# Optimization experiments

Measured on AMD Instinct MI355X. Metric: run time of the kernel, lower is better.

## Reference

```python
import jax, jax.numpy as jnp
import numpy as np

B, C, D, H, W = 4, 128, 16, 16, 16
INNER = 64  # channels // reduction


def setup_inputs() -> dict:
    key = jax.random.key(0)
    ks = jax.random.split(key, 4)
    s = 0.02
    return {
        "x": jax.random.normal(ks[0], (B, C, D, H, W), dtype=jnp.float32),
        "Wq": jax.random.normal(ks[1], (INNER, C), dtype=jnp.float32) * s,
        "bq": jnp.zeros((INNER,), dtype=jnp.float32),
        "Wk": jax.random.normal(ks[2], (INNER, C), dtype=jnp.float32) * s,
        "bk": jnp.zeros((INNER,), dtype=jnp.float32),
        "Wv": jax.random.normal(ks[3], (C, C), dtype=jnp.float32) * s,
        "bv": jnp.zeros((C,), dtype=jnp.float32),
        "gamma": jnp.zeros((1,), dtype=jnp.float32),
    }


def reference(x, Wq, bq, Wk, bk, Wv, bv, gamma):
    b, c, d, h, w = x.shape
    n = d * h * w
    inner = Wq.shape[0]
    scale = inner ** (-0.5)
    xf = x.reshape(b, c, n)  # flatten spatial dims
    # 1x1 Conv3d == per-position channel matmul
    q = jnp.einsum('oc,bcn->bon', Wq, xf) + bq[None, :, None]  # [B, inner, N]
    k = jnp.einsum('oc,bcn->bon', Wk, xf) + bk[None, :, None]  # [B, inner, N]
    v = jnp.einsum('oc,bcn->bon', Wv, xf) + bv[None, :, None]  # [B, C, N]
    # attn[b, n, m] = softmax_m(q[:, :, n] . k[:, :, m] * scale)
    attn = jax.nn.softmax(jnp.einsum('bon,bom->bnm', q, k) * scale, axis=-1)
    # out = v @ attn^T  -> out[b, c, n] = sum_m v[b, c, m] * attn[b, n, m]
    out = jnp.einsum('bcm,bnm->bcn', v, attn).reshape(b, c, d, h, w)
    return x + gamma[0] * out
```

## Files before the change

kernel.cpp:

```cpp
#include <hip/hip_runtime.h>
#include <cstdint>

#define B_ 4
#define C_ 128
#define INNER_ 64
#define N_ 4096
#define SPLITS 12
#define KT 32
#define TT 128

typedef __attribute__((ext_vector_type(8))) short short8;
typedef __attribute__((ext_vector_type(4))) short bf16x4;
typedef __attribute__((ext_vector_type(4))) float f32x4;
typedef __attribute__((ext_vector_type(2))) unsigned u32x2;

typedef const __attribute__((address_space(1))) void* gp_t;
typedef __attribute__((address_space(3))) void* lp_t;

__device__ __forceinline__ short f2bf(float f) {
  unsigned u = __builtin_bit_cast(unsigned, f);
  unsigned r = (u + 0x7FFFu + ((u >> 16) & 1u)) >> 16;
  return (short)r;
}
__device__ __forceinline__ float bf2f(short s) {
  return __builtin_bit_cast(float, ((unsigned)(unsigned short)s) << 16);
}
__device__ __forceinline__ float fexp2(float x) {
#if __has_builtin(__builtin_amdgcn_exp2f)
  return __builtin_amdgcn_exp2f(x);
#else
  return exp2f(x);
#endif
}
__device__ __forceinline__ unsigned pk2(float lo, float hi) {
#if __has_builtin(__builtin_amdgcn_cvt_pk_bf16_f32)
  typedef __attribute__((ext_vector_type(2))) __bf16 bfp;
  bfp v = __builtin_amdgcn_cvt_pk_bf16_f32(lo, hi);
  return __builtin_bit_cast(unsigned, v);
#else
  return (unsigned)(unsigned short)f2bf(lo) | ((unsigned)(unsigned short)f2bf(hi) << 16);
#endif
}

__device__ __forceinline__ f32x4 mfma16(bf16x4 a, bf16x4 b, f32x4 c) {
#if __has_builtin(__builtin_amdgcn_mfma_f32_16x16x16bf16_1k)
  return __builtin_amdgcn_mfma_f32_16x16x16bf16_1k(a, b, c, 0, 0, 0);
#elif __has_builtin(__builtin_amdgcn_mfma_f32_16x16x16_bf16)
  return __builtin_amdgcn_mfma_f32_16x16x16_bf16(a, b, c, 0, 0, 0);
#else
  f32x4 d;
  asm volatile("v_mfma_f32_16x16x16_bf16 %0, %1, %2, %3"
               : "=v"(d) : "v"(a), "v"(b), "v"(c));
  return d;
#endif
}

__global__ __launch_bounds__(256) void pack_kernel(
    const float* __restrict__ Wq, const float* __restrict__ bq,
    const float* __restrict__ Wk, const float* __restrict__ bk,
    const float* __restrict__ Wv, const float* __restrict__ bv,
    short* __restrict__ wp, float* __restrict__ bp)
{
  const int idx = blockIdx.x * 256 + threadIdx.x;
  const int o = idx >> 7, c = idx & 127;
  float v;
  if (o < 64)       v = Wq[o * C_ + c];
  else if (o < 128) v = Wk[(o - 64) * C_ + c];
  else              v = Wv[(o - 128) * C_ + c];
  wp[idx] = f2bf(v);
  if (c == 0)
    bp[o] = (o < 64) ? bq[o] : (o < 128) ? bk[o - 64] : bv[o - 128];
}

__global__ __launch_bounds__(256) void qkv_kernel(
    const float* __restrict__ x, const short* __restrict__ wp,
    const float* __restrict__ bp,
    short* __restrict__ qg, short* __restrict__ kg, short* __restrict__ vg)
{
  __shared__ short xT[32 * 136];
  __shared__ short outb[256 * 40];
  __shared__ float biasL[256];

  const int tid = threadIdx.x;
  const int b   = blockIdx.x >> 7;
  const int n0  = (blockIdx.x & 127) << 5;
  const float QSC = 0.125f * 1.44269504088896340736f;

  biasL[tid] = bp[tid];
  const float* xb = x + (size_t)b * C_ * N_ + n0;
  for (int i = tid; i < 1024; i += 256) {
    const int c = i >> 3, seg = i & 7;
    const float4 v = *(const float4*)&xb[(size_t)c * N_ + seg * 4];
    xT[(seg * 4 + 0) * 136 + c] = f2bf(v.x);
    xT[(seg * 4 + 1) * 136 + c] = f2bf(v.y);
    xT[(seg * 4 + 2) * 136 + c] = f2bf(v.z);
    xT[(seg * 4 + 3) * 136 + c] = f2bf(v.w);
  }
  __syncthreads();

  const int w = tid >> 6, lane = tid & 63, quad = lane >> 4, l16 = lane & 15;

  short8 xf[2][4];
#pragma unroll
  for (int nt = 0; nt < 2; ++nt)
#pragma unroll
    for (int kk = 0; kk < 4; ++kk)
      xf[nt][kk] = *(const short8*)&xT[(nt * 16 + l16) * 136 + kk * 32 + quad * 8];

  if (w < 2) {
    const int obase = w * 64;
    const float osc = (w == 0) ? QSC : 1.0f;
#pragma unroll
    for (int ot = 0; ot < 4; ++ot) {
      const int o = obase + ot * 16 + l16;
      short8 wf[4];
#pragma unroll
      for (int kk = 0; kk < 4; ++kk)
        wf[kk] = *(const short8*)&wp[(size_t)o * 128 + kk * 32 + quad * 8];
      const float bias = biasL[o];
#pragma unroll
      for (int nt = 0; nt < 2; ++nt) {
        f32x4 acc = (f32x4){0.f, 0.f, 0.f, 0.f};
#pragma unroll
        for (int kk = 0; kk < 4; ++kk)
          acc = __builtin_amdgcn_mfma_f32_16x16x32_bf16(xf[nt][kk], wf[kk], acc, 0, 0, 0);
#pragma unroll
        for (int r = 0; r < 4; ++r)
          outb[o * 40 + nt * 16 + quad * 4 + r] = f2bf((acc[r] + bias) * osc);
      }
    }
  } else {
    const int ob2 = (w - 2) * 64;
#pragma unroll
    for (int ot = 0; ot < 4; ++ot) {
      const int orow = 128 + ob2 + ot * 16 + l16;
      short8 wf[4];
#pragma unroll
      for (int kk = 0; kk < 4; ++kk)
        wf[kk] = *(const short8*)&wp[(size_t)orow * 128 + kk * 32 + quad * 8];
#pragma unroll
      for (int nt = 0; nt < 2; ++nt) {
        f32x4 acc = (f32x4){0.f, 0.f, 0.f, 0.f};
#pragma unroll
        for (int kk = 0; kk < 4; ++kk)
          acc = __builtin_amdgcn_mfma_f32_16x16x32_bf16(wf[kk], xf[nt][kk], acc, 0, 0, 0);
#pragma unroll
        for (int r = 0; r < 4; ++r) {
          const int o_r = 128 + ob2 + ot * 16 + quad * 4 + r;
          outb[o_r * 40 + nt * 16 + l16] = f2bf(acc[r] + biasL[o_r]);
        }
      }
    }
  }
  __syncthreads();

  {
    const int n = tid >> 3, oc = tid & 7;
    short8 qv, kv;
#pragma unroll
    for (int j = 0; j < 8; ++j) {
      qv[j] = outb[(oc * 8 + j) * 40 + n];
      kv[j] = outb[(64 + oc * 8 + j) * 40 + n];
    }
    *(short8*)&qg[(((size_t)b * N_ + n0 + n) << 6) + oc * 8] = qv;
    *(short8*)&kg[(((size_t)b * N_ + n0 + n) << 6) + oc * 8] = kv;
  }
  {
    const int T = n0 >> 5;
#pragma unroll
    for (int rep = 0; rep < 2; ++rep) {
      const int idx2 = rep * 256 + tid;
      const int c0  = idx2 & 63;
      const int k4l = idx2 >> 6;
      const bf16x4 lo = *(const bf16x4*)&outb[(128 + 2 * c0) * 40 + k4l * 4];
      const bf16x4 hi = *(const bf16x4*)&outb[(128 + 2 * c0 + 1) * 40 + k4l * 4];
      short8 vv;
#pragma unroll
      for (int j = 0; j < 4; ++j) { vv[j] = lo[j]; vv[4 + j] = hi[j]; }
      const size_t tb = (((size_t)b * 128 + T) * 8 + k4l) * 512 + c0 * 8;
      *(short8*)&vg[tb] = vv;
    }
  }
}

__global__ __launch_bounds__(256, 4) void attn_kernel(
    const short* __restrict__ qb, const short* __restrict__ kb,
    const short* __restrict__ vb,
    short* __restrict__ Opart, float* __restrict__ lbuf)
{
  __shared__ short kbuf[2][2048];
  __shared__ short vbuf[2][4096];

  const int tid = threadIdx.x;
  const int bid = blockIdx.x;
  const int s   = bid % SPLITS;
  const int qt  = (bid / SPLITS) & 31;
  const int b   = bid / (SPLITS * 32);
  const int m0  = qt << 7;
  const int w   = tid >> 6, lane = tid & 63, quad = lane >> 4, l16 = lane & 15;
  const int rbase = m0 + w * 32;

  const int t0  = (s * TT) / SPLITS;
  const int NTs = ((s + 1) * TT) / SPLITS - t0;

  short8 qa[2][2];
#pragma unroll
  for (int mt = 0; mt < 2; ++mt)
#pragma unroll
    for (int kk = 0; kk < 2; ++kk)
      qa[mt][kk] = *(const short8*)&qb[((size_t)b * N_ + rbase + mt * 16 + l16) * 64 + kk * 32 + quad * 8];

  float lsum[2] = {0.f, 0.f};
  f32x4 accO[8][2];
#pragma unroll
  for (int vt = 0; vt < 8; ++vt)
#pragma unroll
    for (int mt = 0; mt < 2; ++mt) accO[vt][mt] = (f32x4){0.f, 0.f, 0.f, 0.f};

  auto dma_tile = [&](int kt, int d) {
    const int T = t0 + kt;
    const short* kbp = kb + (((size_t)b * N_ + T * 32) << 6);
    {
      const int p = w * 64 + lane;
      const int key = p >> 3, jm = (p & 7) ^ (key & 7);
      __builtin_amdgcn_global_load_lds((gp_t)(kbp + (key << 6) + jm * 8),
                                       (lp_t)&kbuf[d][w * 512], 16, 0, 0);
    }
    const short* vtp = vb + ((size_t)b * 128 + T) * 4096;
#pragma unroll
    for (int t = 0; t < 2; ++t) {
      const int p = (w * 2 + t) * 64 + lane;
      __builtin_amdgcn_global_load_lds((gp_t)(vtp + p * 8),
                                       (lp_t)&vbuf[d][(w * 2 + t) * 512], 16, 0, 0);
    }
  };

  dma_tile(0, 0);

  for (int kt = 0; kt < NTs; ++kt) {
    __syncthreads();
    if (kt + 1 < NTs) dma_tile(kt + 1, (kt + 1) & 1);
    const int d = kt & 1;

    bf16x4 pbf[2][2];
#pragma unroll
    for (int ct = 0; ct < 2; ++ct) {
      const short8 kf0 = *(const short8*)&kbuf[d][((ct * 16 + l16) << 6) + ((quad ^ (l16 & 7)) << 3)];
      const short8 kf1 = *(const short8*)&kbuf[d][((ct * 16 + l16) << 6) + (((4 + quad) ^ (l16 & 7)) << 3)];
#pragma unroll
      for (int mt = 0; mt < 2; ++mt) {
        f32x4 st = (f32x4){0.f, 0.f, 0.f, 0.f};
        st = __builtin_amdgcn_mfma_f32_16x16x32_bf16(kf0, qa[mt][0], st, 0, 0, 0);
        st = __builtin_amdgcn_mfma_f32_16x16x32_bf16(kf1, qa[mt][1], st, 0, 0, 0);
        const float p0 = fexp2(st[0]);
        const float p1 = fexp2(st[1]);
        const float p2 = fexp2(st[2]);
        const float p3 = fexp2(st[3]);
        lsum[mt] += (p0 + p1) + (p2 + p3);
        u32x2 pp;
        pp[0] = pk2(p0, p1);
        pp[1] = pk2(p2, p3);
        pbf[ct][mt] = __builtin_bit_cast(bf16x4, pp);
      }
    }

#pragma unroll
    for (int vt = 0; vt < 8; ++vt) {
#pragma unroll
      for (int ct = 0; ct < 2; ++ct) {
        const bf16x4 vf = *(const bf16x4*)&vbuf[d][(ct * 4 + quad) * 512 + (vt * 16 + l16) * 4];
        accO[vt][0] = mfma16(vf, pbf[ct][0], accO[vt][0]);
        accO[vt][1] = mfma16(vf, pbf[ct][1], accO[vt][1]);
      }
    }
  }

#pragma unroll
  for (int mt = 0; mt < 2; ++mt) {
    lsum[mt] += __shfl_xor(lsum[mt], 16);
    lsum[mt] += __shfl_xor(lsum[mt], 32);
  }
  if (quad == 0) {
#pragma unroll
    for (int mt = 0; mt < 2; ++mt)
      lbuf[((size_t)b * SPLITS + s) * N_ + rbase + mt * 16 + l16] = lsum[mt];
  }
#pragma unroll
  for (int vt = 0; vt < 8; ++vt) {
#pragma unroll
    for (int mt = 0; mt < 2; ++mt) {
#pragma unroll
      for (int r = 0; r < 4; ++r) {
        const int ch = vt * 16 + quad * 4 + r;
        Opart[(((size_t)b * SPLITS + s) * C_ + ch) * N_ + rbase + mt * 16 + l16] =
            f2bf(accO[vt][mt][r]);
      }
    }
  }
}

__global__ __launch_bounds__(256) void combine_kernel(
    const float* __restrict__ x, const float* __restrict__ gamma,
    const short* __restrict__ Opart, const float* __restrict__ lbuf,
    float* __restrict__ out)
{
  __shared__ float linvL[64];
  const int tid = threadIdx.x;
  const int b   = blockIdx.x >> 6;
  const int n0  = (blockIdx.x & 63) << 6;

  if (tid < 64) {
    float L = 0.f;
#pragma unroll
    for (int s = 0; s < SPLITS; ++s) L += lbuf[((size_t)b * SPLITS + s) * N_ + n0 + tid];
    linvL[tid] = 1.f / L;
  }
  __syncthreads();

  const float g = gamma[0];
  const int n4 = (tid & 15) * 4, cb = tid >> 4;
#pragma unroll
  for (int cp = 0; cp < 8; ++cp) {
    const int c = cp * 16 + cb;
    float acc[4] = {0.f, 0.f, 0.f, 0.f};
#pragma unroll
    for (int s = 0; s < SPLITS; ++s) {
      const bf16x4 o4 = *(const bf16x4*)&Opart[(((size_t)b * SPLITS + s) * C_ + c) * N_ + n0 + n4];
#pragma unroll
      for (int j = 0; j < 4; ++j) acc[j] += bf2f(o4[j]);
    }
    const size_t xi = ((size_t)b * C_ + c) * N_ + n0 + n4;
    const float4 xv = *(const float4*)&x[xi];
    float4 ov;
    ov.x = xv.x + g * acc[0] * linvL[n4 + 0];
    ov.y = xv.y + g * acc[1] * linvL[n4 + 1];
    ov.z = xv.z + g * acc[2] * linvL[n4 + 2];
    ov.w = xv.w + g * acc[3] * linvL[n4 + 3];
    *(float4*)&out[xi] = ov;
  }
}

extern "C" void kernel_launch(void* const* d_in, const int* in_sizes, int n_in,
                              void* d_out, int out_size, void* d_ws, size_t ws_size,
                              hipStream_t stream) {
  const float* x     = (const float*)d_in[0];
  const float* Wq    = (const float*)d_in[1];
  const float* bq    = (const float*)d_in[2];
  const float* Wk    = (const float*)d_in[3];
  const float* bk    = (const float*)d_in[4];
  const float* Wv    = (const float*)d_in[5];
  const float* bv    = (const float*)d_in[6];
  const float* gamma = (const float*)d_in[7];
  float* out = (float*)d_out;

  short* qb = (short*)d_ws;
  short* kb = qb + (size_t)B_ * N_ * INNER_;
  short* vb = kb + (size_t)B_ * N_ * INNER_;
  short* Opart = vb + (size_t)B_ * C_ * N_;
  float* lbuf  = (float*)(Opart + (size_t)B_ * SPLITS * C_ * N_);
  float* bp    = lbuf + (size_t)B_ * SPLITS * N_;
  short* wp    = (short*)(bp + 256);

  pack_kernel<<<128, 256, 0, stream>>>(Wq, bq, Wk, bk, Wv, bv, wp, bp);
  qkv_kernel<<<B_ * (N_ / 32), 256, 0, stream>>>(x, wp, bp, qb, kb, vb);
  attn_kernel<<<B_ * 32 * SPLITS, 256, 0, stream>>>(qb, kb, vb, Opart, lbuf);
  combine_kernel<<<B_ * (N_ / 64), 256, 0, stream>>>(x, gamma, Opart, lbuf, out);
}
```

Before: 128.6 us.

## Use 16x16x32 bf16 MFMA for PV product with repacked V layout

Replaces pairs of 16x16x16 bf16 MFMAs in the P·V accumulation with single 16x16x32 MFMAs by concatenating the two P fragments and changing the global V tile layout so each lane reads 8 contiguous bf16 values per channel. The projection kernel writes V in the new per-channel contiguous layout. This halves the MFMA instruction count and LDS read instructions in the inner loop, at the cost of wider LDS reads whose bank conflicts may change.

```diff
diff --git a/kernel.cpp b/kernel.cpp
--- a/kernel.cpp
+++ b/kernel.cpp
@@ -13,6 +13,7 @@
 typedef __attribute__((ext_vector_type(4))) short bf16x4;
 typedef __attribute__((ext_vector_type(4))) float f32x4;
 typedef __attribute__((ext_vector_type(2))) unsigned u32x2;
+typedef __attribute__((ext_vector_type(4))) unsigned u32x4;
 
 typedef const __attribute__((address_space(1))) void* gp_t;
 typedef __attribute__((address_space(3))) void* lp_t;
@@ -39,19 +40,6 @@
   return __builtin_bit_cast(unsigned, v);
 #else
   return (unsigned)(unsigned short)f2bf(lo) | ((unsigned)(unsigned short)f2bf(hi) << 16);
-#endif
-}
-
-__device__ __forceinline__ f32x4 mfma16(bf16x4 a, bf16x4 b, f32x4 c) {
-#if __has_builtin(__builtin_amdgcn_mfma_f32_16x16x16bf16_1k)
-  return __builtin_amdgcn_mfma_f32_16x16x16bf16_1k(a, b, c, 0, 0, 0);
-#elif __has_builtin(__builtin_amdgcn_mfma_f32_16x16x16_bf16)
-  return __builtin_amdgcn_mfma_f32_16x16x16_bf16(a, b, c, 0, 0, 0);
-#else
-  f32x4 d;
-  asm volatile("v_mfma_f32_16x16x16_bf16 %0, %1, %2, %3"
-               : "=v"(d) : "v"(a), "v"(b), "v"(c));
-  return d;
 #endif
 }
 
@@ -170,14 +158,13 @@
 #pragma unroll
     for (int rep = 0; rep < 2; ++rep) {
       const int idx2 = rep * 256 + tid;
-      const int c0  = idx2 & 63;
-      const int k4l = idx2 >> 6;
-      const bf16x4 lo = *(const bf16x4*)&outb[(128 + 2 * c0) * 40 + k4l * 4];
-      const bf16x4 hi = *(const bf16x4*)&outb[(128 + 2 * c0 + 1) * 40 + k4l * 4];
+      const int ch = idx2 >> 2, q = idx2 & 3;
+      const bf16x4 lo = *(const bf16x4*)&outb[(128 + ch) * 40 + q * 4];
+      const bf16x4 hi = *(const bf16x4*)&outb[(128 + ch) * 40 + 16 + q * 4];
       short8 vv;
 #pragma unroll
       for (int j = 0; j < 4; ++j) { vv[j] = lo[j]; vv[4 + j] = hi[j]; }
-      const size_t tb = (((size_t)b * 128 + T) * 8 + k4l) * 512 + c0 * 8;
+      const size_t tb = ((size_t)b * 128 + T) * 4096 + (size_t)idx2 * 8;
       *(short8*)&vg[tb] = vv;
     }
   }
@@ -242,7 +229,7 @@
     if (kt + 1 < NTs) dma_tile(kt + 1, (kt + 1) & 1);
     const int d = kt & 1;
 
-    bf16x4 pbf[2][2];
+    u32x2 ppk[2][2];
 #pragma unroll
     for (int ct = 0; ct < 2; ++ct) {
       const short8 kf0 = *(const short8*)&kbuf[d][((ct * 16 + l16) << 6) + ((quad ^ (l16 & 7)) << 3)];
@@ -260,18 +247,21 @@
         u32x2 pp;
         pp[0] = pk2(p0, p1);
         pp[1] = pk2(p2, p3);
-        pbf[ct][mt] = __builtin_bit_cast(bf16x4, pp);
+        ppk[ct][mt] = pp;
       }
     }
+    short8 pcat[2];
+#pragma unroll
+    for (int mt = 0; mt < 2; ++mt) {
+      u32x4 u = (u32x4){ppk[0][mt][0], ppk[0][mt][1], ppk[1][mt][0], ppk[1][mt][1]};
+      pcat[mt] = __builtin_bit_cast(short8, u);
+    }
 
 #pragma unroll
     for (int vt = 0; vt < 8; ++vt) {
-#pragma unroll
-      for (int ct = 0; ct < 2; ++ct) {
-        const bf16x4 vf = *(const bf16x4*)&vbuf[d][(ct * 4 + quad) * 512 + (vt * 16 + l16) * 4];
-        accO[vt][0] = mfma16(vf, pbf[ct][0], accO[vt][0]);
-        accO[vt][1] = mfma16(vf, pbf[ct][1], accO[vt][1]);
-      }
+      const short8 vf = *(const short8*)&vbuf[d][((vt * 16 + l16) << 5) + (quad << 3)];
+      accO[vt][0] = __builtin_amdgcn_mfma_f32_16x16x32_bf16(vf, pcat[0], accO[vt][0], 0, 0, 0);
+      accO[vt][1] = __builtin_amdgcn_mfma_f32_16x16x32_bf16(vf, pcat[1], accO[vt][1], 0, 0, 0);
     }
   }
 
```

Result: no change. 126.7 us (-1.5%).
